# Optimization experiments

Measured on AMD Instinct MI355X. Metric: run time of the kernel, lower is better.

Reference implementation:

```python
import jax, jax.numpy as jnp
import numpy as np

N_NODES = 100000   # num_nodes
N_EDGES = 50000    # num_hyperedges
M = 1600000        # num incidences
D = 64             # hidden_size
N_LAYERS = 1


def setup_inputs() -> dict:
    key = jax.random.key(0)
    k1, k2, k3 = jax.random.split(key, 3)
    x = jax.random.normal(k1, (N_NODES, D), dtype=jnp.float32)
    node_idx = jax.random.randint(k2, (M,), 0, N_NODES, dtype=jnp.int32)
    edge_idx = jax.random.randint(k3, (M,), 0, N_EDGES, dtype=jnp.int32)
    edge_weight = jnp.ones((N_EDGES,), dtype=jnp.float32)
    return {"x": x, "node_idx": node_idx, "edge_idx": edge_idx, "edge_weight": edge_weight}


def _safe_recip(v):
    # 1/v with inf -> 0, matching D[D==inf]=0
    return jnp.where(v > 0, 1.0 / jnp.where(v > 0, v, 1.0), 0.0)


def _hconv(x, node_idx, edge_idx, edge_weight):
    # D[n] = sum over incidences (n,e) of w[e]; B[e] = hyperedge cardinality
    Dn = jax.ops.segment_sum(edge_weight[edge_idx], node_idx, num_segments=N_NODES)
    Dn = _safe_recip(Dn)
    Be = jax.ops.segment_sum(jnp.ones((node_idx.shape[0],), x.dtype), edge_idx, num_segments=N_EDGES)
    Be = _safe_recip(Be)
    # stage 1: nodes -> hyperedges, message = B[e] * x[j]
    edge_feat = jax.ops.segment_sum(x[node_idx] * Be[edge_idx][:, None], edge_idx, num_segments=N_EDGES)
    # stage 2: hyperedges -> nodes, message = D[i] * edge_feat[e]
    out = jax.ops.segment_sum(edge_feat[edge_idx] * Dn[node_idx][:, None], node_idx, num_segments=N_NODES)
    return out


def reference(x, node_idx, edge_idx, edge_weight):
    h = x
    acc = x
    for _ in range(N_LAYERS):
        h = _hconv(h, node_idx, edge_idx, edge_weight)
        acc = acc + h
    return acc / (N_LAYERS + 1)
```

## Files before the change

### kernel.cpp

```cpp
#include <hip/hip_runtime.h>

#define N_NODES 100000
#define N_EDGES 50000
#define N_KEYS  150000
#define M_INC   1600000
#define D_HID   64

#define SUBR    32
#define SUBLEN  50000
#define KPART   65536
#define PN      2
#define PE      1

#define N_TILES_N 25
#define N_TILES_E 13

#define FILL_CHUNKS 49

typedef float v2f __attribute__((ext_vector_type(2)));


__device__ __forceinline__ unsigned enc_fp8x4(float a, float b, float c, float d) {
    unsigned r = 0;
    r = __builtin_amdgcn_cvt_pk_fp8_f32(a, b, r, false);
    r = __builtin_amdgcn_cvt_pk_fp8_f32(c, d, r, true);
    return r;
}

__global__ __launch_bounds__(1024) void count_kernel(
        const int* __restrict__ node_idx, const int* __restrict__ edge_idx,
        unsigned char* __restrict__ rank_n, unsigned char* __restrict__ rank_e,
        unsigned char* __restrict__ cnt_g) {
    __shared__ unsigned int h[KPART / 4];
    int bid = blockIdx.x;
    const int* idx; unsigned char* rk; int p, s, klim, goff;
    if (bid < PN * SUBR) {
        p = bid / SUBR; s = bid % SUBR;
        idx = node_idx; rk = rank_n; klim = N_NODES; goff = 0;
    } else {
        int b2 = bid - PN * SUBR;
        p = b2 / SUBR; s = b2 % SUBR;
        idx = edge_idx; rk = rank_e; klim = N_EDGES; goff = N_NODES;
    }
    int kbase = p * KPART;
    int t = threadIdx.x;
    for (int i = t; i < KPART / 4; i += 1024) h[i] = 0;
    __syncthreads();
    int mbase = s * SUBLEN;
    const int4* src4 = (const int4*)(idx + mbase);
    for (int i = t; i < SUBLEN / 4; i += 1024) {
        int4 v = src4[i];
        int m0 = mbase + i * 4;
        int k;
        k = v.x - kbase;
        if ((unsigned)k < KPART) {
            unsigned sh = 8u * (k & 3);
            unsigned old = atomicAdd(&h[k >> 2], 1u << sh);
            rk[m0 + 0] = (unsigned char)(old >> sh);
        }
        k = v.y - kbase;
        if ((unsigned)k < KPART) {
            unsigned sh = 8u * (k & 3);
            unsigned old = atomicAdd(&h[k >> 2], 1u << sh);
            rk[m0 + 1] = (unsigned char)(old >> sh);
        }
        k = v.z - kbase;
        if ((unsigned)k < KPART) {
            unsigned sh = 8u * (k & 3);
            unsigned old = atomicAdd(&h[k >> 2], 1u << sh);
            rk[m0 + 2] = (unsigned char)(old >> sh);
        }
        k = v.w - kbase;
        if ((unsigned)k < KPART) {
            unsigned sh = 8u * (k & 3);
            unsigned old = atomicAdd(&h[k >> 2], 1u << sh);
            rk[m0 + 3] = (unsigned char)(old >> sh);
        }
    }
    __syncthreads();
    for (int i = t; i < KPART; i += 1024) {
        int key = kbase + i;
        if (key < klim)
            cnt_g[s * N_KEYS + goff + key] =
                (unsigned char)((h[i >> 2] >> (8u * (i & 3))) & 0xFFu);
    }
}

__global__ void totsum_kernel(const unsigned char* __restrict__ cnt_g,
                              int* __restrict__ tot) {
    int key = blockIdx.x * 256 + threadIdx.x;
    if (key < N_KEYS) {
        int base = 0;
#pragma unroll
        for (int k = 0; k < SUBR; k++) base += (int)cnt_g[k * N_KEYS + key];
        tot[key] = base;
    }
}

__global__ void scan_partial_kernel(const int* __restrict__ cnt,
                                    int* __restrict__ pn, int* __restrict__ pe) {
    __shared__ int lds[16];
    int b = blockIdx.x;
    const int* src; int nElem; int tile; int* dst;
    if (b < N_TILES_N) { src = cnt;            nElem = N_NODES; tile = b;             dst = pn; }
    else               { src = cnt + N_NODES;  nElem = N_EDGES; tile = b - N_TILES_N; dst = pe; }
    int t = threadIdx.x;
    int i4 = tile * 1024 + t;
    int sum = 0;
    if (i4 * 4 < nElem) {
        int4 v = ((const int4*)src)[i4];
        sum = v.x + v.y + v.z + v.w;
    }
    for (int off = 1; off < 64; off <<= 1) sum += __shfl_xor(sum, off, 64);
    if ((t & 63) == 0) lds[t >> 6] = sum;
    __syncthreads();
    if (t < 16) {
        int s = lds[t];
        for (int off = 1; off < 16; off <<= 1) s += __shfl_xor(s, off, 64);
        if (t == 0) dst[tile] = s;
    }
}

__global__ void scan_base_kernel(const int* __restrict__ pn, const int* __restrict__ pe,
                                 int* __restrict__ bn, int* __restrict__ be,
                                 int* __restrict__ noff, int* __restrict__ eoff) {
    int w = threadIdx.x >> 6;
    int lane = threadIdx.x & 63;
    if (w == 0) {
        int v = (lane < N_TILES_N) ? pn[lane] : 0;
        int incl = v;
        for (int d = 1; d < 64; d <<= 1) { int u = __shfl_up(incl, d, 64); if (lane >= d) incl += u; }
        if (lane < N_TILES_N) bn[lane] = incl - v;
        if (lane == N_TILES_N - 1) noff[N_NODES] = incl;
    } else {
        int v = (lane < N_TILES_E) ? pe[lane] : 0;
        int incl = v;
        for (int d = 1; d < 64; d <<= 1) { int u = __shfl_up(incl, d, 64); if (lane >= d) incl += u; }
        if (lane < N_TILES_E) be[lane] = incl - v;
        if (lane == N_TILES_E - 1) eoff[N_EDGES] = incl;
    }
}

__global__ void scan_write_kernel(const int* __restrict__ cnt,
                                  const int* __restrict__ bn, const int* __restrict__ be,
                                  int* __restrict__ noff, int* __restrict__ eoff) {
    __shared__ int wsum[16];
    int b = blockIdx.x;
    const int* src; int* dst; int nElem; int tile; int tbase;
    if (b < N_TILES_N) { src = cnt;           dst = noff; nElem = N_NODES; tile = b;             tbase = bn[tile]; }
    else               { src = cnt + N_NODES; dst = eoff; nElem = N_EDGES; tile = b - N_TILES_N; tbase = be[tile]; }
    int t = threadIdx.x;
    int lane = t & 63, w = t >> 6;
    int i4 = tile * 1024 + t;
    int4 c = make_int4(0, 0, 0, 0);
    bool valid = (i4 * 4 < nElem);
    if (valid) c = ((const int4*)src)[i4];
    int tsum = c.x + c.y + c.z + c.w;
    int incl = tsum;
    for (int d = 1; d < 64; d <<= 1) { int u = __shfl_up(incl, d, 64); if (lane >= d) incl += u; }
    if (lane == 63) wsum[w] = incl;
    __syncthreads();
    if (t < 16) {
        int v = wsum[t];
        int wi = v;
        for (int d = 1; d < 16; d <<= 1) { int u = __shfl_up(wi, d, 64); if (t >= d) wi += u; }
        wsum[t] = wi - v;
    }
    __syncthreads();
    int ex = tbase + wsum[w] + incl - tsum;
    if (valid) {
        int4 o;
        o.x = ex; o.y = ex + c.x; o.z = o.y + c.y; o.w = o.z + c.z;
        ((int4*)dst)[i4] = o;
    }
}

__global__ void absprefix_kernel(const unsigned char* __restrict__ cnt_g,
                                 const int* __restrict__ noff, const int* __restrict__ eoff,
                                 unsigned int* __restrict__ absb) {
    int key = blockIdx.x * 256 + threadIdx.x;
    if (key < N_KEYS) {
        unsigned base = (key < N_NODES) ? (unsigned)noff[key]
                                        : (unsigned)eoff[key - N_NODES];
#pragma unroll
        for (int k = 0; k < SUBR; k++) {
            absb[k * N_KEYS + key] = base;
            base += (unsigned)cnt_g[k * N_KEYS + key];
        }
    }
}

__global__ __launch_bounds__(256) void fill_kernel(
        const int* __restrict__ node_idx, const int* __restrict__ edge_idx,
        const unsigned char* __restrict__ rank_n, const unsigned char* __restrict__ rank_e,
        const unsigned int* __restrict__ absb,
        unsigned short* __restrict__ node_csr, int* __restrict__ edge_csr) {
    int b = blockIdx.x;
    int x = b & 7;
    int r = b >> 3;
    int g = r / FILL_CHUNKS;
    int c = r % FILL_CHUNKS;
    int s = x + 8 * g;
    int li = c * 256 + (int)threadIdx.x;
    if (li < SUBLEN / 4) {
        int q = s * (SUBLEN / 4) + li;
        const unsigned int* ab = absb + s * N_KEYS;
        int4 nv = ((const int4*)node_idx)[q];
        int4 ev = ((const int4*)edge_idx)[q];
        uchar4 rn = ((const uchar4*)rank_n)[q];
        uchar4 re = ((const uchar4*)rank_e)[q];
        node_csr[ab[nv.x] + (unsigned)rn.x] = (unsigned short)ev.x;
        node_csr[ab[nv.y] + (unsigned)rn.y] = (unsigned short)ev.y;
        node_csr[ab[nv.z] + (unsigned)rn.z] = (unsigned short)ev.z;
        node_csr[ab[nv.w] + (unsigned)rn.w] = (unsigned short)ev.w;
        edge_csr[ab[N_NODES + ev.x] + (unsigned)re.x] = nv.x;
        edge_csr[ab[N_NODES + ev.y] + (unsigned)re.y] = nv.y;
        edge_csr[ab[N_NODES + ev.z] + (unsigned)re.z] = nv.z;
        edge_csr[ab[N_NODES + ev.w] + (unsigned)re.w] = nv.w;
    }
}

__global__ void cvt_kernel(const float* __restrict__ x, uint2* __restrict__ xh) {
    int i = blockIdx.x * 256 + threadIdx.x;
    if (i < (N_NODES * D_HID) / 8) {
        const float4* x4 = (const float4*)x;
        float4 a = x4[i * 2], b = x4[i * 2 + 1];
        uint2 o;
        o.x = enc_fp8x4(a.x, a.y, a.z, a.w);
        o.y = enc_fp8x4(b.x, b.y, b.z, b.w);
        xh[i] = o;
    }
}

__global__ void stage1_kernel(const int* __restrict__ eoff, const int* __restrict__ ecsr,
                              const uint2* __restrict__ xh, uint2* __restrict__ ef) {
    int wid = (blockIdx.x * 256 + threadIdx.x) >> 6;
    if (wid >= N_EDGES) return;
    int lane = threadIdx.x & 63;
    int group = lane >> 3;
    int gl = lane & 7;
    int s = eoff[wid], t = eoff[wid + 1];
    float acc[8] = {0.f, 0.f, 0.f, 0.f, 0.f, 0.f, 0.f, 0.f};
    for (int m = s + group; m < t; m += 8) {
        int mi = ecsr[m];
        uint2 v = xh[mi * 8 + gl];
        v2f d0 = __builtin_amdgcn_cvt_pk_f32_fp8(v.x, false);
        v2f d1 = __builtin_amdgcn_cvt_pk_f32_fp8(v.x, true);
        v2f d2 = __builtin_amdgcn_cvt_pk_f32_fp8(v.y, false);
        v2f d3 = __builtin_amdgcn_cvt_pk_f32_fp8(v.y, true);
        acc[0] += d0.x; acc[1] += d0.y; acc[2] += d1.x; acc[3] += d1.y;
        acc[4] += d2.x; acc[5] += d2.y; acc[6] += d3.x; acc[7] += d3.y;
    }
    for (int off = 8; off < 64; off <<= 1)
#pragma unroll
        for (int i = 0; i < 8; i++) acc[i] += __shfl_xor(acc[i], off, 64);
    if (group == 0) {
        int card = t - s;
        float ber = (card > 0) ? (1.0f / (float)card) : 0.f;
        uint2 o;
        o.x = enc_fp8x4(acc[0] * ber, acc[1] * ber, acc[2] * ber, acc[3] * ber);
        o.y = enc_fp8x4(acc[4] * ber, acc[5] * ber, acc[6] * ber, acc[7] * ber);
        ef[(size_t)wid * 8 + gl] = o;
    }
}

__global__ void stage2_kernel(const int* __restrict__ noff, const unsigned short* __restrict__ ncsr,
                              const uint2* __restrict__ ef, const float* __restrict__ ew,
                              const float* __restrict__ x, float* __restrict__ out) {
    int wid = (blockIdx.x * 256 + threadIdx.x) >> 6;
    if (wid >= N_NODES) return;
    int lane = threadIdx.x & 63;
    int group = lane >> 3;
    int gl = lane & 7;
    int s = noff[wid], t = noff[wid + 1];
    float acc[8] = {0.f, 0.f, 0.f, 0.f, 0.f, 0.f, 0.f, 0.f};
    float dn = 0.f;
    for (int m = s + group; m < t; m += 8) {
        int mi = (int)ncsr[m];
        float w = ew[mi];
        if (gl == 0) dn += w;
        uint2 v = ef[mi * 8 + gl];
        v2f d0 = __builtin_amdgcn_cvt_pk_f32_fp8(v.x, false);
        v2f d1 = __builtin_amdgcn_cvt_pk_f32_fp8(v.x, true);
        v2f d2 = __builtin_amdgcn_cvt_pk_f32_fp8(v.y, false);
        v2f d3 = __builtin_amdgcn_cvt_pk_f32_fp8(v.y, true);
        acc[0] += d0.x; acc[1] += d0.y; acc[2] += d1.x; acc[3] += d1.y;
        acc[4] += d2.x; acc[5] += d2.y; acc[6] += d3.x; acc[7] += d3.y;
    }
    for (int off = 1; off < 64; off <<= 1) dn += __shfl_xor(dn, off, 64);
    for (int off = 8; off < 64; off <<= 1)
#pragma unroll
        for (int i = 0; i < 8; i++) acc[i] += __shfl_xor(acc[i], off, 64);
    if (group == 0) {
        float dnr = (dn > 0.f) ? (1.0f / dn) : 0.f;
        const float4* x4 = (const float4*)x;
        float4* o4 = (float4*)out;
        float4 a = x4[(size_t)wid * 16 + gl * 2];
        float4 b = x4[(size_t)wid * 16 + gl * 2 + 1];
        float4 ra, rb2;
        ra.x = 0.5f * (a.x + dnr * acc[0]);
        ra.y = 0.5f * (a.y + dnr * acc[1]);
        ra.z = 0.5f * (a.z + dnr * acc[2]);
        ra.w = 0.5f * (a.w + dnr * acc[3]);
        rb2.x = 0.5f * (b.x + dnr * acc[4]);
        rb2.y = 0.5f * (b.y + dnr * acc[5]);
        rb2.z = 0.5f * (b.z + dnr * acc[6]);
        rb2.w = 0.5f * (b.w + dnr * acc[7]);
        o4[(size_t)wid * 16 + gl * 2] = ra;
        o4[(size_t)wid * 16 + gl * 2 + 1] = rb2;
    }
}

extern "C" void kernel_launch(void* const* d_in, const int* in_sizes, int n_in,
                              void* d_out, int out_size, void* d_ws, size_t ws_size,
                              hipStream_t stream) {
    const float* x        = (const float*)d_in[0];
    const int*   node_idx = (const int*)d_in[1];
    const int*   edge_idx = (const int*)d_in[2];
    const float* ew       = (const float*)d_in[3];
    float* out = (float*)d_out;

    char* ws = (char*)d_ws;
    unsigned char*  rank_n   = (unsigned char*)(ws + 0);
    unsigned char*  rank_e   = (unsigned char*)(ws + 1600000);
    int*            noff     = (int*)(ws + 3200000);
    int*            eoff     = (int*)(ws + 3600016);
    unsigned short* node_csr = (unsigned short*)(ws + 3800032);
    int*            edge_csr = (int*)(ws + 7000032);
    unsigned int*   absb     = (unsigned int*)(ws + 13400032);
    unsigned char*  cnt_g = (unsigned char*)(ws + 3800032);
    int*            tot   = (int*)(ws + 32600032);
    int*            pn    = (int*)(ws + 33200032);
    int*            pe    = pn + 32;
    int*            bn    = pn + 64;
    int*            be    = pn + 96;
    uint2*          ef    = (uint2*)(ws + 0);
    uint2*          xh    = (uint2*)(ws + 13400032);

    count_kernel<<<(PN + PE) * SUBR, 1024, 0, stream>>>(node_idx, edge_idx, rank_n, rank_e, cnt_g);
    totsum_kernel<<<(N_KEYS + 255) / 256, 256, 0, stream>>>(cnt_g, tot);
    scan_partial_kernel<<<N_TILES_N + N_TILES_E, 1024, 0, stream>>>(tot, pn, pe);
    scan_base_kernel<<<1, 128, 0, stream>>>(pn, pe, bn, be, noff, eoff);
    scan_write_kernel<<<N_TILES_N + N_TILES_E, 1024, 0, stream>>>(tot, bn, be, noff, eoff);
    absprefix_kernel<<<(N_KEYS + 255) / 256, 256, 0, stream>>>(cnt_g, noff, eoff, absb);
    fill_kernel<<<8 * (SUBR / 8) * FILL_CHUNKS, 256, 0, stream>>>(node_idx, edge_idx, rank_n, rank_e,
                                                                  absb, node_csr, edge_csr);
    cvt_kernel<<<((N_NODES * D_HID / 8) + 255) / 256, 256, 0, stream>>>(x, xh);
    stage1_kernel<<<(N_EDGES * 64 + 255) / 256, 256, 0, stream>>>(eoff, edge_csr, xh, ef);
    stage2_kernel<<<(N_NODES * 64 + 255) / 256, 256, 0, stream>>>(noff, node_csr, ef, ew, x, out);
}
```

Baseline: 245.3 us.

## Map eight segments per wavefront with shuffled index broadcast in gather stages

Both gather stages now give each wavefront eight edges or nodes, one per 8-lane group, instead of one segment per wavefront. Each group loads eight CSR indices cooperatively and broadcasts them with shuffles, so no cross-group reduction is needed and every group writes its own output row. The aim is to remove the reduction shuffles, cut the idle group-0-only epilogue, and raise useful work per wave. The cost is a serial inner loop per segment and load imbalance between groups whose segments differ in length.

```diff
diff --git a/kernel.cpp b/kernel.cpp
--- a/kernel.cpp
+++ b/kernel.cpp
@@ -234,81 +234,85 @@
 
 __global__ void stage1_kernel(const int* __restrict__ eoff, const int* __restrict__ ecsr,
                               const uint2* __restrict__ xh, uint2* __restrict__ ef) {
-    int wid = (blockIdx.x * 256 + threadIdx.x) >> 6;
-    if (wid >= N_EDGES) return;
+    int wq = (blockIdx.x * 256 + threadIdx.x) >> 6;
+    int e0 = wq * 8;
+    if (e0 >= N_EDGES) return;
     int lane = threadIdx.x & 63;
-    int group = lane >> 3;
+    int g = lane >> 3;
     int gl = lane & 7;
-    int s = eoff[wid], t = eoff[wid + 1];
+    int e = e0 + g;
+    int s = eoff[e], t = eoff[e + 1];
     float acc[8] = {0.f, 0.f, 0.f, 0.f, 0.f, 0.f, 0.f, 0.f};
-    for (int m = s + group; m < t; m += 8) {
-        int mi = ecsr[m];
-        uint2 v = xh[mi * 8 + gl];
-        v2f d0 = __builtin_amdgcn_cvt_pk_f32_fp8(v.x, false);
-        v2f d1 = __builtin_amdgcn_cvt_pk_f32_fp8(v.x, true);
-        v2f d2 = __builtin_amdgcn_cvt_pk_f32_fp8(v.y, false);
-        v2f d3 = __builtin_amdgcn_cvt_pk_f32_fp8(v.y, true);
-        acc[0] += d0.x; acc[1] += d0.y; acc[2] += d1.x; acc[3] += d1.y;
-        acc[4] += d2.x; acc[5] += d2.y; acc[6] += d3.x; acc[7] += d3.y;
-    }
-    for (int off = 8; off < 64; off <<= 1)
-#pragma unroll
-        for (int i = 0; i < 8; i++) acc[i] += __shfl_xor(acc[i], off, 64);
-    if (group == 0) {
-        int card = t - s;
-        float ber = (card > 0) ? (1.0f / (float)card) : 0.f;
-        uint2 o;
-        o.x = enc_fp8x4(acc[0] * ber, acc[1] * ber, acc[2] * ber, acc[3] * ber);
-        o.y = enc_fp8x4(acc[4] * ber, acc[5] * ber, acc[6] * ber, acc[7] * ber);
-        ef[(size_t)wid * 8 + gl] = o;
-    }
+    int gbase = lane & 56;
+    for (int base = s; base < t; base += 8) {
+        int idx_l = (base + gl < t) ? ecsr[base + gl] : 0;
+        int cnt = t - base; if (cnt > 8) cnt = 8;
+        for (int j = 0; j < cnt; j++) {
+            int mi = __shfl(idx_l, gbase + j, 64);
+            uint2 v = xh[mi * 8 + gl];
+            v2f d0 = __builtin_amdgcn_cvt_pk_f32_fp8(v.x, false);
+            v2f d1 = __builtin_amdgcn_cvt_pk_f32_fp8(v.x, true);
+            v2f d2 = __builtin_amdgcn_cvt_pk_f32_fp8(v.y, false);
+            v2f d3 = __builtin_amdgcn_cvt_pk_f32_fp8(v.y, true);
+            acc[0] += d0.x; acc[1] += d0.y; acc[2] += d1.x; acc[3] += d1.y;
+            acc[4] += d2.x; acc[5] += d2.y; acc[6] += d3.x; acc[7] += d3.y;
+        }
+    }
+    int card = t - s;
+    float ber = (card > 0) ? (1.0f / (float)card) : 0.f;
+    uint2 o;
+    o.x = enc_fp8x4(acc[0] * ber, acc[1] * ber, acc[2] * ber, acc[3] * ber);
+    o.y = enc_fp8x4(acc[4] * ber, acc[5] * ber, acc[6] * ber, acc[7] * ber);
+    ef[(size_t)e * 8 + gl] = o;
 }
 
 __global__ void stage2_kernel(const int* __restrict__ noff, const unsigned short* __restrict__ ncsr,
                               const uint2* __restrict__ ef, const float* __restrict__ ew,
                               const float* __restrict__ x, float* __restrict__ out) {
-    int wid = (blockIdx.x * 256 + threadIdx.x) >> 6;
-    if (wid >= N_NODES) return;
+    int wq = (blockIdx.x * 256 + threadIdx.x) >> 6;
+    int n0 = wq * 8;
+    if (n0 >= N_NODES) return;
     int lane = threadIdx.x & 63;
-    int group = lane >> 3;
+    int g = lane >> 3;
     int gl = lane & 7;
-    int s = noff[wid], t = noff[wid + 1];
+    int n = n0 + g;
+    int s = noff[n], t = noff[n + 1];
     float acc[8] = {0.f, 0.f, 0.f, 0.f, 0.f, 0.f, 0.f, 0.f};
     float dn = 0.f;
-    for (int m = s + group; m < t; m += 8) {
-        int mi = (int)ncsr[m];
-        float w = ew[mi];
-        if (gl == 0) dn += w;
-        uint2 v = ef[mi * 8 + gl];
-        v2f d0 = __builtin_amdgcn_cvt_pk_f32_fp8(v.x, false);
-        v2f d1 = __builtin_amdgcn_cvt_pk_f32_fp8(v.x, true);
-        v2f d2 = __builtin_amdgcn_cvt_pk_f32_fp8(v.y, false);
-        v2f d3 = __builtin_amdgcn_cvt_pk_f32_fp8(v.y, true);
-        acc[0] += d0.x; acc[1] += d0.y; acc[2] += d1.x; acc[3] += d1.y;
-        acc[4] += d2.x; acc[5] += d2.y; acc[6] += d3.x; acc[7] += d3.y;
-    }
-    for (int off = 1; off < 64; off <<= 1) dn += __shfl_xor(dn, off, 64);
-    for (int off = 8; off < 64; off <<= 1)
-#pragma unroll
-        for (int i = 0; i < 8; i++) acc[i] += __shfl_xor(acc[i], off, 64);
-    if (group == 0) {
-        float dnr = (dn > 0.f) ? (1.0f / dn) : 0.f;
-        const float4* x4 = (const float4*)x;
-        float4* o4 = (float4*)out;
-        float4 a = x4[(size_t)wid * 16 + gl * 2];
-        float4 b = x4[(size_t)wid * 16 + gl * 2 + 1];
-        float4 ra, rb2;
-        ra.x = 0.5f * (a.x + dnr * acc[0]);
-        ra.y = 0.5f * (a.y + dnr * acc[1]);
-        ra.z = 0.5f * (a.z + dnr * acc[2]);
-        ra.w = 0.5f * (a.w + dnr * acc[3]);
-        rb2.x = 0.5f * (b.x + dnr * acc[4]);
-        rb2.y = 0.5f * (b.y + dnr * acc[5]);
-        rb2.z = 0.5f * (b.z + dnr * acc[6]);
-        rb2.w = 0.5f * (b.w + dnr * acc[7]);
-        o4[(size_t)wid * 16 + gl * 2] = ra;
-        o4[(size_t)wid * 16 + gl * 2 + 1] = rb2;
-    }
+    int gbase = lane & 56;
+    for (int base = s; base < t; base += 8) {
+        bool lv = (base + gl < t);
+        int idx_l = lv ? (int)ncsr[base + gl] : 0;
+        if (lv) dn += ew[idx_l];
+        int cnt = t - base; if (cnt > 8) cnt = 8;
+        for (int j = 0; j < cnt; j++) {
+            int mi = __shfl(idx_l, gbase + j, 64);
+            uint2 v = ef[mi * 8 + gl];
+            v2f d0 = __builtin_amdgcn_cvt_pk_f32_fp8(v.x, false);
+            v2f d1 = __builtin_amdgcn_cvt_pk_f32_fp8(v.x, true);
+            v2f d2 = __builtin_amdgcn_cvt_pk_f32_fp8(v.y, false);
+            v2f d3 = __builtin_amdgcn_cvt_pk_f32_fp8(v.y, true);
+            acc[0] += d0.x; acc[1] += d0.y; acc[2] += d1.x; acc[3] += d1.y;
+            acc[4] += d2.x; acc[5] += d2.y; acc[6] += d3.x; acc[7] += d3.y;
+        }
+    }
+    for (int off = 1; off < 8; off <<= 1) dn += __shfl_xor(dn, off, 64);
+    float dnr = (dn > 0.f) ? (1.0f / dn) : 0.f;
+    const float4* x4 = (const float4*)x;
+    float4* o4 = (float4*)out;
+    float4 a = x4[(size_t)n * 16 + gl * 2];
+    float4 b = x4[(size_t)n * 16 + gl * 2 + 1];
+    float4 ra, rb2;
+    ra.x = 0.5f * (a.x + dnr * acc[0]);
+    ra.y = 0.5f * (a.y + dnr * acc[1]);
+    ra.z = 0.5f * (a.z + dnr * acc[2]);
+    ra.w = 0.5f * (a.w + dnr * acc[3]);
+    rb2.x = 0.5f * (b.x + dnr * acc[4]);
+    rb2.y = 0.5f * (b.y + dnr * acc[5]);
+    rb2.z = 0.5f * (b.z + dnr * acc[6]);
+    rb2.w = 0.5f * (b.w + dnr * acc[7]);
+    o4[(size_t)n * 16 + gl * 2] = ra;
+    o4[(size_t)n * 16 + gl * 2 + 1] = rb2;
 }
 
 extern "C" void kernel_launch(void* const* d_in, const int* in_sizes, int n_in,
@@ -346,6 +350,6 @@
     fill_kernel<<<8 * (SUBR / 8) * FILL_CHUNKS, 256, 0, stream>>>(node_idx, edge_idx, rank_n, rank_e,
                                                                   absb, node_csr, edge_csr);
     cvt_kernel<<<((N_NODES * D_HID / 8) + 255) / 256, 256, 0, stream>>>(x, xh);
-    stage1_kernel<<<(N_EDGES * 64 + 255) / 256, 256, 0, stream>>>(eoff, edge_csr, xh, ef);
-    stage2_kernel<<<(N_NODES * 64 + 255) / 256, 256, 0, stream>>>(noff, node_csr, ef, ew, x, out);
-}
+    stage1_kernel<<<(N_EDGES / 8 * 64 + 255) / 256, 256, 0, stream>>>(eoff, edge_csr, xh, ef);
+    stage2_kernel<<<(N_NODES / 8 * 64 + 255) / 256, 256, 0, stream>>>(noff, node_csr, ef, ew, x, out);
+}
```

After: 225.3 us, median of 2. -8.1%, faster.
